# Optimization experiments

Measured on AMD Instinct MI355X. Metric: run time of the kernel, lower is better.

The kernel has to match this reference:

```python
import jax, jax.numpy as jnp
import numpy as np
import math

# dims: batch, tgt_len, img_feat, wordvec, heads, vocab, layers, ffn
N, T, D, W, H, V, L, FF = 8, 512, 1024, 512, 4, 32000, 2, 2048
NULL = 0  # padding_idx -> zero embedding row


def _pos_encoding(max_len, dim):
    pos = jnp.arange(max_len, dtype=jnp.float32)[:, None]
    j = jnp.arange(dim)[None, :]
    je = (j - (j % 2)).astype(jnp.float32)
    ang = pos * jnp.power(10000.0, -je / dim)
    return jnp.where(j % 2 == 0, jnp.sin(ang), jnp.cos(ang))  # (max_len, dim)


def setup_inputs() -> dict:
    key = jax.random.key(0)
    ks = iter(jax.random.split(key, 80))

    def nrm(shape):
        return jax.random.normal(next(ks), shape, jnp.float32) * 0.02

    inp = {}
    inp["features"] = jax.random.normal(next(ks), (N, D), jnp.float32)
    inp["captions"] = jax.random.randint(next(ks), (N, T), 0, V)
    emb = nrm((V, W)).at[NULL].set(0.0)  # padding_idx row zeroed
    inp["emb"] = emb
    inp["pe"] = _pos_encoding(T, W)
    inp["vis_w"] = nrm((D, W)); inp["vis_b"] = jnp.zeros((W,), jnp.float32)
    for p in ["sa", "ca"]:
        for q in ["q", "k", "v", "o"]:
            inp[f"{p}_w{q}"] = nrm((L, W, W))
            inp[f"{p}_b{q}"] = jnp.zeros((L, W), jnp.float32)
    inp["ff1_w"] = nrm((L, W, FF)); inp["ff1_b"] = jnp.zeros((L, FF), jnp.float32)
    inp["ff2_w"] = nrm((L, FF, W)); inp["ff2_b"] = jnp.zeros((L, W), jnp.float32)
    for i in (1, 2, 3):
        inp[f"ln{i}_w"] = jnp.ones((L, W), jnp.float32)
        inp[f"ln{i}_b"] = jnp.zeros((L, W), jnp.float32)
    inp["out_w"] = nrm((W, V)); inp["out_b"] = jnp.zeros((V,), jnp.float32)
    return inp


def _layer_norm(x, w, b):
    m = x.mean(-1, keepdims=True)
    v = ((x - m) ** 2).mean(-1, keepdims=True)
    return (x - m) / jnp.sqrt(v + 1e-5) * w + b


def _mha(qx, kx, vx, wq, bq, wk, bk, wv, bv, wo, bo, mask):
    n, s, e = qx.shape
    t = kx.shape[1]
    d = e // H
    q = (qx @ wq + bq).reshape(n, s, H, d)
    k = (kx @ wk + bk).reshape(n, t, H, d)
    v = (vx @ wv + bv).reshape(n, t, H, d)
    a = jnp.einsum("nshd,nthd->nhst", q, k) / math.sqrt(d)  # (N,H,S,T)
    if mask is not None:
        a = jnp.where(mask, a, -jnp.inf)
    e_ = jax.nn.softmax(a, axis=-1)
    y = jnp.einsum("nhst,nthd->nshd", e_, v).reshape(n, s, e)
    return y @ wo + bo


def reference(features, captions, emb, pe, vis_w, vis_b,
              sa_wq, sa_bq, sa_wk, sa_bk, sa_wv, sa_bv, sa_wo, sa_bo,
              ca_wq, ca_bq, ca_wk, ca_bk, ca_wv, ca_bv, ca_wo, ca_bo,
              ff1_w, ff1_b, ff2_w, ff2_b,
              ln1_w, ln1_b, ln2_w, ln2_b, ln3_w, ln3_b, out_w, out_b):
    memory = (features @ vis_w + vis_b)[:, None, :]  # (N,1,W)
    t_len = captions.shape[1]
    x = emb[captions] + pe[None, :t_len, :]  # (N,T,W)
    mask = jnp.tril(jnp.ones((t_len, t_len), bool))  # causal tgt_mask
    for l in range(L):
        t2 = _mha(x, x, x, sa_wq[l], sa_bq[l], sa_wk[l], sa_bk[l],
                  sa_wv[l], sa_bv[l], sa_wo[l], sa_bo[l], mask)
        x = _layer_norm(x + t2, ln1_w[l], ln1_b[l])
        t2 = _mha(x, memory, memory, ca_wq[l], ca_bq[l], ca_wk[l], ca_bk[l],
                  ca_wv[l], ca_bv[l], ca_wo[l], ca_bo[l], None)
        x = _layer_norm(x + t2, ln2_w[l], ln2_b[l])
        t2 = jax.nn.relu(x @ ff1_w[l] + ff1_b[l]) @ ff2_w[l] + ff2_b[l]
        x = _layer_norm(x + t2, ln3_w[l], ln3_b[l])
    return x @ out_w + out_b  # (N,T,V)
```

## Files before the change

### kernel.cpp

```cpp
#include <hip/hip_runtime.h>
#include <math.h>

#define WDIM   512
#define TLEN   512
#define NBATCH 8
#define NHEADS 4
#define DHEAD  128
#define VOCAB  32000
#define NLAY   2
#define FFDIM  2048
#define DFEAT  1024
#define NT     (NBATCH * TLEN)
#define QKVW   (3 * WDIM)

typedef unsigned short u16;
typedef __attribute__((ext_vector_type(8))) short bf16x8;
typedef __attribute__((ext_vector_type(4))) float f32x4;

__device__ inline u16 f2bf(float f) {
    union { float f; unsigned u; } v; v.f = f;
    unsigned r = v.u + 0x7fffu + ((v.u >> 16) & 1u);
    return (u16)(r >> 16);
}
__device__ inline u16 to_bf(float f) { return f2bf(f); }
__device__ inline u16 to_bf(u16 v)  { return v; }

__global__ __launch_bounds__(256)
void cvt_kernel(const float* __restrict__ s, u16* __restrict__ d, int n)
{
    int i = blockIdx.x * 256 + threadIdx.x;
    if (i < n) d[i] = f2bf(s[i]);
}

__global__ __launch_bounds__(256)
void concat_bias_kernel(const float* __restrict__ bq, const float* __restrict__ bk,
                        const float* __restrict__ bv, float* __restrict__ dst)
{
    int i = blockIdx.x * 256 + threadIdx.x;
    if (i >= NLAY * QKVW) return;
    int l = i / QKVW, j = i - l * QKVW;
    float v = (j < WDIM) ? bq[l * WDIM + j]
            : (j < 2 * WDIM) ? bk[l * WDIM + j - WDIM]
            : bv[l * WDIM + j - 2 * WDIM];
    dst[i] = v;
}

template<typename T>
__global__ __launch_bounds__(256)
void transpose_cvt_kernel(const T* __restrict__ src, int lds_, long ssn, long ssh,
                          u16* __restrict__ dst, int ldd, long dsn, long dsh,
                          int HH)
{
    int z = blockIdx.z;
    int zn = z / HH, zh = z - zn * HH;
    src += (long)zn * ssn + (long)zh * ssh;
    dst += (long)zn * dsn + (long)zh * dsh;
    __shared__ T tile[32][33];
    int n0 = blockIdx.x * 32, k0 = blockIdx.y * 32;
    int tx = threadIdx.x & 31, ty = threadIdx.x >> 5;
    #pragma unroll
    for (int i = 0; i < 32; i += 8)
        tile[ty + i][tx] = src[(long)(k0 + ty + i) * lds_ + n0 + tx];
    __syncthreads();
    #pragma unroll
    for (int i = 0; i < 32; i += 8)
        dst[(long)(n0 + ty + i) * ldd + k0 + tx] = to_bf(tile[tx][ty + i]);
}

__global__ __launch_bounds__(128)
void embed_kernel(const int* __restrict__ captions, const float* __restrict__ emb,
                  const float* __restrict__ pe, float* __restrict__ x, u16* __restrict__ xb)
{
    int r = blockIdx.x;
    int t = r % TLEN;
    int cap = captions[r];
    const float4* e4 = (const float4*)(emb + (long)cap * WDIM);
    const float4* p4 = (const float4*)(pe + (long)t * WDIM);
    float4 a = e4[threadIdx.x], b = p4[threadIdx.x];
    float4 o = make_float4(a.x + b.x, a.y + b.y, a.z + b.z, a.w + b.w);
    ((float4*)(x + (long)r * WDIM))[threadIdx.x] = o;
    ushort4 ob = make_ushort4(f2bf(o.x), f2bf(o.y), f2bf(o.z), f2bf(o.w));
    ((ushort4*)(xb + (long)r * WDIM))[threadIdx.x] = ob;
}

#define GBM 128
#define GBN 128
#define GBK 32

template<int RELU, int NTST, int CAUSAL>
__global__ __launch_bounds__(256)
void mfma_gemm_kernel(const u16* __restrict__ A, int lda, long sAn, long sAh,
                      const u16* __restrict__ B, int ldb, long sBn, long sBh,
                      float* __restrict__ C, u16* __restrict__ Cb, int ldc, long sCn, long sCh,
                      const float* __restrict__ bias, long sbias,
                      int M, int N, int K, int HH, float alpha)
{
    int z = blockIdx.z;
    int zn = z / HH, zh = z - zn * HH;
    A += (long)zn * sAn + (long)zh * sAh;
    B += (long)zn * sBn + (long)zh * sBh;
    long coff = (long)zn * sCn + (long)zh * sCh;
    if (bias) bias += (long)zn * sbias;

    int nwg  = gridDim.x * gridDim.y;
    int orig = blockIdx.y * gridDim.x + blockIdx.x;
    int q = nwg >> 3, r = nwg & 7, xcd = orig & 7, rest = orig >> 3;
    int nw = (xcd < r ? xcd * (q + 1) : r * (q + 1) + (xcd - r) * q) + rest;
    int bx = nw / gridDim.y, by = nw - bx * gridDim.y;
    int bm = by * GBM, bn = bx * GBN;

    if (CAUSAL && bn >= bm + GBM) return;

    __shared__ u16 As[2][GBM * GBK];
    __shared__ u16 Bs[2][GBN * GBK];

    int tid = threadIdx.x;
    int w = tid >> 6, lane = tid & 63;
    int wr = w >> 1, wc = w & 1;
    int lrow = lane & 15, kgrp = lane >> 4;

    int c0row = tid >> 2, c0ko = (tid & 3) << 3;
    long ldsOff = (size_t)(w * 64) * 8;

    auto STAGE = [&](int buf, int ks) {
        int k0 = ks * GBK;
        #pragma unroll
        for (int i = 0; i < 2; i++) {
            int row = c0row + i * 64;
            int gr = bm + row; if (gr >= M) gr = M - 1;
            const u16* srcA = A + (long)gr * lda + k0 + c0ko;
            u16* dstA = &As[buf][ldsOff + (size_t)i * 256 * 8];
            __builtin_amdgcn_global_load_lds((const __attribute__((address_space(1))) void*)srcA,
                                             (__attribute__((address_space(3))) void*)dstA, 16, 0, 0);
            const u16* srcB = B + (long)(bn + row) * ldb + k0 + c0ko;
            u16* dstB = &Bs[buf][ldsOff + (size_t)i * 256 * 8];
            __builtin_amdgcn_global_load_lds((const __attribute__((address_space(1))) void*)srcB,
                                             (__attribute__((address_space(3))) void*)dstB, 16, 0, 0);
        }
    };

    f32x4 acc[4][4] = {};
    int nsteps = K / GBK;

    STAGE(0, 0);

    for (int ks = 0; ks < nsteps; ks++) {
        int cur = ks & 1;
        if (ks + 1 < nsteps) {
            STAGE(cur ^ 1, ks + 1);
            asm volatile("s_waitcnt vmcnt(4)" ::: "memory");
        } else {
            asm volatile("s_waitcnt vmcnt(0)" ::: "memory");
        }
        __builtin_amdgcn_sched_barrier(0);
        __builtin_amdgcn_s_barrier();
        __builtin_amdgcn_sched_barrier(0);
        bf16x8 av[4], bv[4];
        #pragma unroll
        for (int m = 0; m < 4; m++)
            av[m] = *(const bf16x8*)&As[cur][(wr * 64 + m * 16 + lrow) * GBK + kgrp * 8];
        #pragma unroll
        for (int n = 0; n < 4; n++)
            bv[n] = *(const bf16x8*)&Bs[cur][(wc * 64 + n * 16 + lrow) * GBK + kgrp * 8];
        #pragma unroll
        for (int m = 0; m < 4; m++)
            #pragma unroll
            for (int n = 0; n < 4; n++)
                acc[m][n] = __builtin_amdgcn_mfma_f32_16x16x32_bf16(av[m], bv[n], acc[m][n], 0, 0, 0);
        __builtin_amdgcn_sched_barrier(0);
        __builtin_amdgcn_s_barrier();
        __builtin_amdgcn_sched_barrier(0);
    }

    if (NTST) {
        __syncthreads();
        float* ls = (float*)&As[0][0];
        C += coff;
        #pragma unroll
        for (int pass = 0; pass < 4; pass++) {
            if (wr == (pass >> 1)) {
                #pragma unroll
                for (int m2 = 0; m2 < 2; m2++) {
                    int m = (pass & 1) * 2 + m2;
                    #pragma unroll
                    for (int n = 0; n < 4; n++) {
                        int gc = wc * 64 + n * 16 + lrow;
                        float bvv = bias ? bias[bn + gc] : 0.f;
                        #pragma unroll
                        for (int r2 = 0; r2 < 4; r2++) {
                            float v2 = acc[m][n][r2] * alpha + bvv;
                            if (RELU) v2 = fmaxf(v2, 0.f);
                            ls[(m2 * 16 + kgrp * 4 + r2) * 128 + gc] = v2;
                        }
                    }
                }
            }
            __syncthreads();
            #pragma unroll
            for (int i = 0; i < 4; i++) {
                int j = tid + i * 256;
                int row = j >> 5, cg = j & 31;
                int gr = bm + pass * 32 + row;
                if (gr < M) {
                    f32x4 v4 = *(const f32x4*)&ls[row * 128 + cg * 4];
                    __builtin_nontemporal_store(v4, (f32x4*)&C[(long)gr * ldc + bn + cg * 4]);
                }
            }
            __syncthreads();
        }
        return;
    }

    if (C)  C  += coff;
    if (Cb) Cb += coff;
    #pragma unroll
    for (int m = 0; m < 4; m++) {
        int rb = bm + wr * 64 + m * 16 + kgrp * 4;
        #pragma unroll
        for (int n = 0; n < 4; n++) {
            int gc = bn + wc * 64 + n * 16 + lrow;
            float bvv = bias ? bias[gc] : 0.f;
            #pragma unroll
            for (int r2 = 0; r2 < 4; r2++) {
                int gr = rb + r2;
                if (gr < M) {
                    float v2 = acc[m][n][r2] * alpha + bvv;
                    if (RELU) v2 = fmaxf(v2, 0.f);
                    if (C)  C[(long)gr * ldc + gc]  = v2;
                    if (Cb) Cb[(long)gr * ldc + gc] = f2bf(v2);
                }
            }
        }
    }
}

__global__ __launch_bounds__(256)
void softmax_causal_kernel(const float* __restrict__ scores, u16* __restrict__ pb)
{
    long row = blockIdx.x;
    int s = (int)(row % TLEN);
    const float* p = scores + row * TLEN;
    u16* o = pb + row * TLEN;
    int tid = threadIdx.x;
    float v0 = p[tid], v1 = p[tid + 256];
    bool m0 = (tid <= s), m1 = (tid + 256 <= s);
    __shared__ float red[256];
    float mx = fmaxf(m0 ? v0 : -INFINITY, m1 ? v1 : -INFINITY);
    red[tid] = mx; __syncthreads();
    for (int off = 128; off > 0; off >>= 1) {
        if (tid < off) red[tid] = fmaxf(red[tid], red[tid + off]);
        __syncthreads();
    }
    mx = red[0]; __syncthreads();
    float e0 = m0 ? expf(v0 - mx) : 0.f;
    float e1 = m1 ? expf(v1 - mx) : 0.f;
    red[tid] = e0 + e1; __syncthreads();
    for (int off = 128; off > 0; off >>= 1) {
        if (tid < off) red[tid] += red[tid + off];
        __syncthreads();
    }
    float inv = 1.f / red[0];
    o[tid]       = f2bf(e0 * inv);
    o[tid + 256] = f2bf(e1 * inv);
}

__device__ inline void ln_pass(float& v0, float& v1, const float* __restrict__ w,
                               const float* __restrict__ b, float* red, int tid)
{
    red[tid] = v0 + v1; __syncthreads();
    for (int off = 128; off > 0; off >>= 1) {
        if (tid < off) red[tid] += red[tid + off];
        __syncthreads();
    }
    float mean = red[0] * (1.f / WDIM); __syncthreads();
    float d0 = v0 - mean, d1 = v1 - mean;
    red[tid] = d0 * d0 + d1 * d1; __syncthreads();
    for (int off = 128; off > 0; off >>= 1) {
        if (tid < off) red[tid] += red[tid + off];
        __syncthreads();
    }
    float rstd = 1.f / sqrtf(red[0] * (1.f / WDIM) + 1e-5f);
    __syncthreads();
    v0 = d0 * rstd * w[tid] + b[tid];
    v1 = d1 * rstd * w[tid + 256] + b[tid + 256];
}

__global__ __launch_bounds__(256)
void add_ln_kernel(float* __restrict__ x, u16* __restrict__ xb,
                   const float* __restrict__ t2,
                   const float* __restrict__ w, const float* __restrict__ b)
{
    long r = blockIdx.x;
    float* xr = x + r * WDIM;
    u16* xbr = xb + r * WDIM;
    const float* tr = t2 + r * WDIM;
    int tid = threadIdx.x;
    float v0 = xr[tid] + tr[tid];
    float v1 = xr[tid + 256] + tr[tid + 256];
    __shared__ float red[256];
    ln_pass(v0, v1, w, b, red, tid);
    xr[tid] = v0;        xr[tid + 256] = v1;
    xbr[tid] = f2bf(v0); xbr[tid + 256] = f2bf(v1);
}

__global__ __launch_bounds__(256)
void add_ln2_kernel(float* __restrict__ x, u16* __restrict__ xb,
                    const float* __restrict__ t2, const float* __restrict__ cav,
                    const float* __restrict__ w1, const float* __restrict__ b1,
                    const float* __restrict__ w2, const float* __restrict__ b2)
{
    long r = blockIdx.x;
    float* xr = x + r * WDIM;
    u16* xbr = xb + r * WDIM;
    const float* tr = t2 + r * WDIM;
    const float* cr = cav + (r / TLEN) * WDIM;
    int tid = threadIdx.x;
    float v0 = xr[tid] + tr[tid];
    float v1 = xr[tid + 256] + tr[tid + 256];
    __shared__ float red[256];
    ln_pass(v0, v1, w1, b1, red, tid);
    __syncthreads();
    v0 += cr[tid]; v1 += cr[tid + 256];
    ln_pass(v0, v1, w2, b2, red, tid);
    xr[tid] = v0;        xr[tid + 256] = v1;
    xbr[tid] = f2bf(v0); xbr[tid + 256] = f2bf(v1);
}

extern "C" void kernel_launch(void* const* d_in, const int* in_sizes, int n_in,
                              void* d_out, int out_size, void* d_ws, size_t ws_size,
                              hipStream_t stream)
{
    const float* features = (const float*)d_in[0];
    const int*   captions = (const int*)  d_in[1];
    const float* emb      = (const float*)d_in[2];
    const float* pe       = (const float*)d_in[3];
    const float* vis_w    = (const float*)d_in[4];
    const float* vis_b    = (const float*)d_in[5];
    const float* sa_wq    = (const float*)d_in[6];
    const float* sa_bq    = (const float*)d_in[7];
    const float* sa_wk    = (const float*)d_in[8];
    const float* sa_bk    = (const float*)d_in[9];
    const float* sa_wv    = (const float*)d_in[10];
    const float* sa_bv    = (const float*)d_in[11];
    const float* sa_wo    = (const float*)d_in[12];
    const float* sa_bo    = (const float*)d_in[13];
    const float* ca_wv    = (const float*)d_in[18];
    const float* ca_bv    = (const float*)d_in[19];
    const float* ca_wo    = (const float*)d_in[20];
    const float* ca_bo    = (const float*)d_in[21];
    const float* ff1_w    = (const float*)d_in[22];
    const float* ff1_b    = (const float*)d_in[23];
    const float* ff2_w    = (const float*)d_in[24];
    const float* ff2_b    = (const float*)d_in[25];
    const float* ln1_w    = (const float*)d_in[26];
    const float* ln1_b    = (const float*)d_in[27];
    const float* ln2_w    = (const float*)d_in[28];
    const float* ln2_b    = (const float*)d_in[29];
    const float* ln3_w    = (const float*)d_in[30];
    const float* ln3_b    = (const float*)d_in[31];
    const float* out_w    = (const float*)d_in[32];
    const float* out_b    = (const float*)d_in[33];

    char* p = (char*)d_ws;
    auto alloc = [&](size_t bytes) { char* r = p; p += (bytes + 255) & ~(size_t)255; return r; };
    float* x    = (float*)alloc((size_t)NT * WDIM * 4);
    float* t2   = (float*)alloc((size_t)NT * WDIM * 4);
    float* memb = (float*)alloc((size_t)NBATCH * WDIM * 4);
    float* cav  = (float*)alloc((size_t)NLAY * NBATCH * WDIM * 4);
    char*  reg1 = alloc((size_t)NBATCH * NHEADS * TLEN * TLEN * 4);
    float* scores = (float*)reg1;
    u16*   yb     = (u16*)reg1;
    u16*   hb     = (u16*)reg1;
    u16* xb    = (u16*)alloc((size_t)NT * WDIM * 2);
    u16* qkvb  = (u16*)alloc((size_t)NT * QKVW * 2);
    u16* vtb   = (u16*)alloc((size_t)NT * WDIM * 2);
    u16* pb    = (u16*)alloc((size_t)NBATCH * NHEADS * TLEN * TLEN * 2);
    u16* featb = (u16*)alloc((size_t)NBATCH * DFEAT * 2);
    u16* membf = (u16*)alloc((size_t)NBATCH * WDIM * 2);
    u16* cvb   = (u16*)alloc((size_t)NLAY * NBATCH * WDIM * 2);
    float* qkv_bias = (float*)alloc((size_t)NLAY * QKVW * 4);
    u16* vis_wT = (u16*)alloc((size_t)WDIM * DFEAT * 2);
    u16* qkvT   = (u16*)alloc((size_t)NLAY * QKVW * WDIM * 2);
    u16* sa_woT = (u16*)alloc((size_t)NLAY * WDIM * WDIM * 2);
    u16* ca_wvT = (u16*)alloc((size_t)NLAY * WDIM * WDIM * 2);
    u16* ca_woT = (u16*)alloc((size_t)NLAY * WDIM * WDIM * 2);
    u16* ff1T   = (u16*)alloc((size_t)NLAY * WDIM * FFDIM * 2);
    u16* ff2T   = (u16*)alloc((size_t)NLAY * FFDIM * WDIM * 2);
    u16* out_wT = (u16*)alloc((size_t)WDIM * VOCAB * 2);

    auto gemm = [&](const u16* A, int lda, long sAn, long sAh,
                    const u16* B, int ldb, long sBn, long sBh,
                    float* C, u16* Cb, int ldc, long sCn, long sCh,
                    const float* bias, long sbias, int M, int N, int K, int HH, int batch,
                    float alpha, int mode)
    {
        dim3 g(N / GBN, (M + GBM - 1) / GBM, batch), blk(256);
        if (mode == 2)
            mfma_gemm_kernel<0, 1, 0><<<g, blk, 0, stream>>>(A, lda, sAn, sAh, B, ldb, sBn, sBh,
                                                             C, Cb, ldc, sCn, sCh, bias, sbias, M, N, K, HH, alpha);
        else if (mode == 1)
            mfma_gemm_kernel<1, 0, 0><<<g, blk, 0, stream>>>(A, lda, sAn, sAh, B, ldb, sBn, sBh,
                                                             C, Cb, ldc, sCn, sCh, bias, sbias, M, N, K, HH, alpha);
        else if (mode == 3)
            mfma_gemm_kernel<0, 0, 1><<<g, blk, 0, stream>>>(A, lda, sAn, sAh, B, ldb, sBn, sBh,
                                                             C, Cb, ldc, sCn, sCh, bias, sbias, M, N, K, HH, alpha);
        else
            mfma_gemm_kernel<0, 0, 0><<<g, blk, 0, stream>>>(A, lda, sAn, sAh, B, ldb, sBn, sBh,
                                                             C, Cb, ldc, sCn, sCh, bias, sbias, M, N, K, HH, alpha);
    };
    auto transposeF = [&](const float* src, int lds_, long ssn, long ssh,
                          u16* dst, int ldd, long dsn, long dsh,
                          int K, int N, int batch, int HH)
    {
        dim3 g(N / 32, K / 32, batch), blk(256);
        transpose_cvt_kernel<float><<<g, blk, 0, stream>>>(src, lds_, ssn, ssh, dst, ldd, dsn, dsh, HH);
    };
    auto transposeB = [&](const u16* src, int lds_, long ssn, long ssh,
                          u16* dst, int ldd, long dsn, long dsh,
                          int K, int N, int batch, int HH)
    {
        dim3 g(N / 32, K / 32, batch), blk(256);
        transpose_cvt_kernel<u16><<<g, blk, 0, stream>>>(src, lds_, ssn, ssh, dst, ldd, dsn, dsh, HH);
    };

    cvt_kernel<<<(NBATCH * DFEAT + 255) / 256, 256, 0, stream>>>(features, featb, NBATCH * DFEAT);
    concat_bias_kernel<<<(NLAY * QKVW + 255) / 256, 256, 0, stream>>>(sa_bq, sa_bk, sa_bv, qkv_bias);
    transposeF(vis_w, WDIM, 0, 0, vis_wT, DFEAT, 0, 0, DFEAT, WDIM, 1, 1);
    transposeF(sa_wq, WDIM, (long)WDIM * WDIM, 0, qkvT,                WDIM, (long)QKVW * WDIM, 0, WDIM, WDIM, NLAY, 1);
    transposeF(sa_wk, WDIM, (long)WDIM * WDIM, 0, qkvT + (long)WDIM * WDIM,     WDIM, (long)QKVW * WDIM, 0, WDIM, WDIM, NLAY, 1);
    transposeF(sa_wv, WDIM, (long)WDIM * WDIM, 0, qkvT + (long)2 * WDIM * WDIM, WDIM, (long)QKVW * WDIM, 0, WDIM, WDIM, NLAY, 1);
    transposeF(sa_wo, WDIM, (long)WDIM * WDIM, 0, sa_woT, WDIM, (long)WDIM * WDIM, 0, WDIM, WDIM, NLAY, 1);
    transposeF(ca_wv, WDIM, (long)WDIM * WDIM, 0, ca_wvT, WDIM, (long)WDIM * WDIM, 0, WDIM, WDIM, NLAY, 1);
    transposeF(ca_wo, WDIM, (long)WDIM * WDIM, 0, ca_woT, WDIM, (long)WDIM * WDIM, 0, WDIM, WDIM, NLAY, 1);
    transposeF(ff1_w, FFDIM, (long)WDIM * FFDIM, 0, ff1T, WDIM, (long)FFDIM * WDIM, 0, WDIM, FFDIM, NLAY, 1);
    transposeF(ff2_w, WDIM, (long)FFDIM * WDIM, 0, ff2T, FFDIM, (long)WDIM * FFDIM, 0, FFDIM, WDIM, NLAY, 1);
    transposeF(out_w, VOCAB, 0, 0, out_wT, WDIM, 0, 0, WDIM, VOCAB, 1, 1);

    gemm(featb, DFEAT, 0, 0, vis_wT, DFEAT, 0, 0, memb, membf, WDIM, 0, 0,
         vis_b, 0, NBATCH, WDIM, DFEAT, 1, 1, 1.f, 0);
    embed_kernel<<<NT, 128, 0, stream>>>(captions, emb, pe, x, xb);

    gemm(membf, WDIM, 0, 0, ca_wvT, WDIM, (long)WDIM * WDIM, 0,
         nullptr, cvb, WDIM, (long)NBATCH * WDIM, 0,
         ca_bv, WDIM, NBATCH, WDIM, WDIM, 1, NLAY, 1.f, 0);
    gemm(cvb, WDIM, (long)NBATCH * WDIM, 0, ca_woT, WDIM, (long)WDIM * WDIM, 0,
         cav, nullptr, WDIM, (long)NBATCH * WDIM, 0,
         ca_bo, WDIM, NBATCH, WDIM, WDIM, 1, NLAY, 1.f, 0);

    const float iscale = 1.f / sqrtf((float)DHEAD);
    const long TQ = (long)TLEN * QKVW;
    const long TW = (long)TLEN * WDIM;
    const long TT = (long)TLEN * TLEN;
    for (int l = 0; l < NLAY; l++) {
        long wo  = (long)l * WDIM * WDIM;
        long bo_ = (long)l * WDIM;
        gemm(xb, WDIM, 0, 0, qkvT + (long)l * QKVW * WDIM, WDIM, 0, 0,
             nullptr, qkvb, QKVW, 0, 0, qkv_bias + (long)l * QKVW, 0,
             NT, QKVW, WDIM, 1, 1, 1.f, 0);
        transposeB(qkvb + 2 * WDIM, QKVW, TQ, DHEAD,
                   vtb, TLEN, (long)NHEADS * DHEAD * TLEN, (long)DHEAD * TLEN,
                   TLEN, DHEAD, NBATCH * NHEADS, NHEADS);
        gemm(qkvb, QKVW, TQ, DHEAD, qkvb + WDIM, QKVW, TQ, DHEAD,
             scores, nullptr, TLEN, (long)NHEADS * TT, TT,
             nullptr, 0, TLEN, TLEN, DHEAD, NHEADS, NBATCH * NHEADS, iscale, 3);
        softmax_causal_kernel<<<NBATCH * NHEADS * TLEN, 256, 0, stream>>>(scores, pb);
        gemm(pb, TLEN, (long)NHEADS * TT, TT,
             vtb, TLEN, (long)NHEADS * DHEAD * TLEN, (long)DHEAD * TLEN,
             nullptr, yb, WDIM, TW, DHEAD,
             nullptr, 0, TLEN, DHEAD, TLEN, NHEADS, NBATCH * NHEADS, 1.f, 0);
        gemm(yb, WDIM, 0, 0, sa_woT + wo, WDIM, 0, 0, t2, nullptr, WDIM, 0, 0,
             sa_bo + bo_, 0, NT, WDIM, WDIM, 1, 1, 1.f, 0);
        add_ln2_kernel<<<NT, 256, 0, stream>>>(x, xb, t2, cav + (long)l * NBATCH * WDIM,
                                               ln1_w + bo_, ln1_b + bo_, ln2_w + bo_, ln2_b + bo_);
        gemm(xb, WDIM, 0, 0, ff1T + (long)l * FFDIM * WDIM, WDIM, 0, 0,
             nullptr, hb, FFDIM, 0, 0, ff1_b + (long)l * FFDIM, 0,
             NT, FFDIM, WDIM, 1, 1, 1.f, 1);
        gemm(hb, FFDIM, 0, 0, ff2T + (long)l * WDIM * FFDIM, FFDIM, 0, 0,
             t2, nullptr, WDIM, 0, 0, ff2_b + bo_, 0, NT, WDIM, FFDIM, 1, 1, 1.f, 0);
        add_ln_kernel<<<NT, 256, 0, stream>>>(x, xb, t2, ln3_w + bo_, ln3_b + bo_);
    }
    gemm(xb, WDIM, 0, 0, out_wT, WDIM, 0, 0, (float*)d_out, nullptr, VOCAB, 0, 0,
         out_b, 0, NT, VOCAB, WDIM, 1, 1, 1.f, 2);
}
```

Baseline: 736.7 us.

## Load GEMM operands directly from global into registers, dropping LDS staging

Replaces the double-buffered LDS staging (global_load_lds plus barriers) in the GEMM kernel with per-lane direct global loads into registers, software-pipelined two k-steps deep. This removes the LDS round trip and the workgroup barriers per k-step. In exchange, each wave now loads its own A and B fragments separately, so rows shared across waves are fetched redundantly from global/L2 with less coalesced 16-byte accesses per row. It also raises register pressure from holding two fragment sets.

```diff
diff --git a/kernel.cpp b/kernel.cpp
--- a/kernel.cpp
+++ b/kernel.cpp
@@ -111,70 +111,54 @@
 
     if (CAUSAL && bn >= bm + GBM) return;
 
-    __shared__ u16 As[2][GBM * GBK];
-    __shared__ u16 Bs[2][GBN * GBK];
+    __shared__ float ls[32 * 128];
 
     int tid = threadIdx.x;
     int w = tid >> 6, lane = tid & 63;
     int wr = w >> 1, wc = w & 1;
     int lrow = lane & 15, kgrp = lane >> 4;
-
-    int c0row = tid >> 2, c0ko = (tid & 3) << 3;
-    long ldsOff = (size_t)(w * 64) * 8;
-
-    auto STAGE = [&](int buf, int ks) {
-        int k0 = ks * GBK;
-        #pragma unroll
-        for (int i = 0; i < 2; i++) {
-            int row = c0row + i * 64;
-            int gr = bm + row; if (gr >= M) gr = M - 1;
-            const u16* srcA = A + (long)gr * lda + k0 + c0ko;
-            u16* dstA = &As[buf][ldsOff + (size_t)i * 256 * 8];
-            __builtin_amdgcn_global_load_lds((const __attribute__((address_space(1))) void*)srcA,
-                                             (__attribute__((address_space(3))) void*)dstA, 16, 0, 0);
-            const u16* srcB = B + (long)(bn + row) * ldb + k0 + c0ko;
-            u16* dstB = &Bs[buf][ldsOff + (size_t)i * 256 * 8];
-            __builtin_amdgcn_global_load_lds((const __attribute__((address_space(1))) void*)srcB,
-                                             (__attribute__((address_space(3))) void*)dstB, 16, 0, 0);
-        }
-    };
+    int ko = kgrp * 8;
+
+    const u16* Arow[4];
+    const u16* Brow[4];
+    #pragma unroll
+    for (int m = 0; m < 4; m++) {
+        int gr = bm + wr * 64 + m * 16 + lrow; if (gr >= M) gr = M - 1;
+        Arow[m] = A + (long)gr * lda;
+    }
+    #pragma unroll
+    for (int n = 0; n < 4; n++)
+        Brow[n] = B + (long)(bn + wc * 64 + n * 16 + lrow) * ldb;
 
     f32x4 acc[4][4] = {};
     int nsteps = K / GBK;
 
-    STAGE(0, 0);
-
-    for (int ks = 0; ks < nsteps; ks++) {
-        int cur = ks & 1;
-        if (ks + 1 < nsteps) {
-            STAGE(cur ^ 1, ks + 1);
-            asm volatile("s_waitcnt vmcnt(4)" ::: "memory");
-        } else {
-            asm volatile("s_waitcnt vmcnt(0)" ::: "memory");
-        }
-        __builtin_amdgcn_sched_barrier(0);
-        __builtin_amdgcn_s_barrier();
-        __builtin_amdgcn_sched_barrier(0);
-        bf16x8 av[4], bv[4];
+    bf16x8 a0[4], b0[4], a1[4], b1[4];
+
+    auto LOAD = [&](int ks, bf16x8* av, bf16x8* bv) {
+        int k0 = ks * GBK + ko;
         #pragma unroll
-        for (int m = 0; m < 4; m++)
-            av[m] = *(const bf16x8*)&As[cur][(wr * 64 + m * 16 + lrow) * GBK + kgrp * 8];
+        for (int m = 0; m < 4; m++) av[m] = *(const bf16x8*)(Arow[m] + k0);
         #pragma unroll
-        for (int n = 0; n < 4; n++)
-            bv[n] = *(const bf16x8*)&Bs[cur][(wc * 64 + n * 16 + lrow) * GBK + kgrp * 8];
+        for (int n = 0; n < 4; n++) bv[n] = *(const bf16x8*)(Brow[n] + k0);
+    };
+    auto MF = [&](bf16x8* av, bf16x8* bv) {
         #pragma unroll
         for (int m = 0; m < 4; m++)
             #pragma unroll
             for (int n = 0; n < 4; n++)
                 acc[m][n] = __builtin_amdgcn_mfma_f32_16x16x32_bf16(av[m], bv[n], acc[m][n], 0, 0, 0);
-        __builtin_amdgcn_sched_barrier(0);
-        __builtin_amdgcn_s_barrier();
-        __builtin_amdgcn_sched_barrier(0);
+    };
+
+    LOAD(0, a0, b0);
+    for (int ks = 0; ks < nsteps; ks += 2) {
+        if (ks + 1 < nsteps) LOAD(ks + 1, a1, b1);
+        MF(a0, b0);
+        if (ks + 2 < nsteps) LOAD(ks + 2, a0, b0);
+        if (ks + 1 < nsteps) MF(a1, b1);
     }
 
     if (NTST) {
-        __syncthreads();
-        float* ls = (float*)&As[0][0];
         C += coff;
         #pragma unroll
         for (int pass = 0; pass < 4; pass++) {
```

Measured after the change: 1.164 ms. 1.58x slower.
